# Kernel tuning notes

Measured on AMD Instinct MI355X. Metric: run time of the kernel, lower is better.

## Reference

```python
import jax, jax.numpy as jnp
import numpy as np

T, B, F, H, A, MH = 512, 256, 512, 128, 8, 64


def setup_inputs() -> dict:
    key = jax.random.key(0)
    ks = jax.random.split(key, 14)
    s = 0.05
    return {
        "x": jax.random.normal(ks[0], (T, B, F), dtype=jnp.float32),
        "done": (jax.random.uniform(ks[1], (T, B)) < 0.1).astype(jnp.float32),
        "h0": jnp.zeros((B, H), dtype=jnp.float32),
        "c0": jnp.zeros((B, H), dtype=jnp.float32),
        "W_ih": jax.random.normal(ks[2], (4 * H, F), dtype=jnp.float32) * s,
        "W_hh": jax.random.normal(ks[3], (4 * H, H), dtype=jnp.float32) * s,
        "b_ih": jnp.zeros((4 * H,), dtype=jnp.float32),
        "b_hh": jnp.zeros((4 * H,), dtype=jnp.float32),
        "W_p1": jax.random.normal(ks[4], (H, MH), dtype=jnp.float32) * s,
        "b_p1": jnp.zeros((MH,), dtype=jnp.float32),
        "W_p2": jax.random.normal(ks[5], (MH, A), dtype=jnp.float32) * s,
        "b_p2": jnp.zeros((A,), dtype=jnp.float32),
        "W_v1": jax.random.normal(ks[6], (H, MH), dtype=jnp.float32) * s,
        "b_v1": jnp.zeros((MH,), dtype=jnp.float32),
        "W_v2": jax.random.normal(ks[7], (MH, 1), dtype=jnp.float32) * s,
        "b_v2": jnp.zeros((1,), dtype=jnp.float32),
    }


def _masked_lstm(x, done, h0, c0, W_ih, W_hh, b_ih, b_hh):
    # Per-timestep LSTM with done-mask reset, as in MemoryAgent.remember().
    def step(carry, inp):
        h, c = carry
        xt, dt = inp  # xt: [B,F], dt: [B]
        m = (1.0 - dt)[:, None]
        h = h * m
        c = c * m
        gates = xt @ W_ih.T + b_ih + h @ W_hh.T + b_hh  # [B,4H]
        i, f, g, o = jnp.split(gates, 4, axis=-1)  # PyTorch gate order i,f,g,o
        i = jax.nn.sigmoid(i)
        f = jax.nn.sigmoid(f)
        g = jnp.tanh(g)
        o = jax.nn.sigmoid(o)
        c = f * c + i * g
        h = o * jnp.tanh(c)
        return (h, c), h

    (hT, cT), hs = jax.lax.scan(step, (h0, c0), (x, done))
    return hs.reshape(-1, h0.shape[-1]), hT, cT  # [T*B,H]


def reference(x, done, h0, c0, W_ih, W_hh, b_ih, b_hh,
              W_p1, b_p1, W_p2, b_p2, W_v1, b_v1, W_v2, b_v2):
    hseq, hT, cT = _masked_lstm(x, done, h0, c0, W_ih, W_hh, b_ih, b_hh)
    logits = jnp.tanh(hseq @ W_p1 + b_p1) @ W_p2 + b_p2  # [T*B,A]
    v = jnp.tanh(hseq @ W_v1 + b_v1) @ W_v2 + b_v2        # [T*B,1]
    out = jnp.concatenate([logits, v], axis=1)            # [T*B,A+1]
    return out, hT, cT
```

## Files before the change

### kernel.cpp

```cpp
#include <hip/hip_runtime.h>
#include <stdint.h>

#define T_  512
#define B_  256
#define F_  512
#define H_  128
#define MH_ 64
#define A_  8
#define OUT0 1179648
#define OUT1 32768

typedef float f32x4 __attribute__((ext_vector_type(4)));
typedef __bf16 bfrag8 __attribute__((ext_vector_type(8)));
typedef unsigned short u16;
typedef unsigned int u32;

#define WS_GATES 0u
#define WS_HSEQ  134217728u
#define WS_WIH   167772160u
#define WS_WHH   168296448u
#define WS_WP1   168427520u
#define WS_WV1   168443904u

__device__ inline u16 f2bf(float f) {
  union { float f; u32 u; } v; v.f = f;
  u32 u = v.u;
  u32 r = (u + 0x7FFFu + ((u >> 16) & 1u)) >> 16;
  return (u16)r;
}
__device__ inline float bf2f(u16 b) {
  union { u32 u; float f; } v; v.u = ((u32)b) << 16;
  return v.f;
}

__device__ inline float fexp2(float x) {
#if __has_builtin(__builtin_amdgcn_exp2f)
  return __builtin_amdgcn_exp2f(x);
#else
  return exp2f(x);
#endif
}
__device__ inline float frcp(float x) {
#if __has_builtin(__builtin_amdgcn_rcpf)
  return __builtin_amdgcn_rcpf(x);
#else
  return 1.0f / x;
#endif
}
__device__ inline float sig_(float x) {
  return frcp(1.0f + fexp2(-1.44269504f * x));
}
__device__ inline float tanh_(float x) {
  x = fminf(30.0f, fmaxf(-30.0f, x));
  float t = fexp2(2.88539008f * x);
  return (t - 1.0f) * frcp(t + 1.0f);
}
__device__ inline float sel4(f32x4 a, int q) {
  float s01 = (q & 1) ? a[1] : a[0];
  float s23 = (q & 1) ? a[3] : a[2];
  return (q & 2) ? s23 : s01;
}

__device__ inline f32x4 mfma16(bfrag8 a, bfrag8 b, f32x4 c) {
  return __builtin_amdgcn_mfma_f32_16x16x32_bf16(a, b, c, 0, 0, 0);
}

__device__ inline void gld16(const void* g, void* l) {
  __builtin_amdgcn_global_load_lds((const __attribute__((address_space(1))) void*)g,
                                   (__attribute__((address_space(3))) void*)l, 16, 0, 0);
}

__global__ __launch_bounds__(256) void k0_prep(const float* __restrict__ W_ih,
                                               const float* __restrict__ W_hh,
                                               const float* __restrict__ W_p1,
                                               const float* __restrict__ W_v1,
                                               u16* __restrict__ wih_swz,
                                               u16* __restrict__ whh_bf,
                                               u16* __restrict__ wp1s,
                                               u16* __restrict__ wv1s) {
  int idx = blockIdx.x * 256 + threadIdx.x;
  if (idx < 262144) {
    int i = idx & 7, L = (idx >> 3) & 63, kb = (idx >> 9) & 15, nt = idx >> 13;
    wih_swz[idx] = f2bf(W_ih[(nt * 16 + (L & 15)) * 512 + kb * 32 + ((L >> 4) << 3) + i]);
  } else if (idx < 262144 + 65536) {
    int j = idx - 262144;
    whh_bf[j] = f2bf(W_hh[j]);
  } else if (idx < 262144 + 65536 + 8192) {
    int j = idx - (262144 + 65536);
    int i = j & 7, L = (j >> 3) & 63, kb = (j >> 9) & 3, nt = j >> 11;
    wp1s[j] = f2bf(W_p1[(kb * 32 + ((L >> 4) << 3) + i) * 64 + nt * 16 + (L & 15)]);
  } else if (idx < 262144 + 65536 + 16384) {
    int j = idx - (262144 + 65536 + 8192);
    int i = j & 7, L = (j >> 3) & 63, kb = (j >> 9) & 3, nt = j >> 11;
    wv1s[j] = f2bf(W_v1[(kb * 32 + ((L >> 4) << 3) + i) * 64 + nt * 16 + (L & 15)]);
  }
}

__global__ __launch_bounds__(512) void k1_gates(const float* __restrict__ x,
                                                const u16* __restrict__ wih_swz,
                                                const float* __restrict__ b_ih,
                                                const float* __restrict__ b_hh,
                                                u16* __restrict__ gates) {
  __shared__ __align__(16) u16 Abuf[16 * 64 * 8];
  __shared__ __align__(16) u16 Bbuf[64 * 64 * 8];
  const int tid = threadIdx.x;
  const int lane = tid & 63;
  const int w = tid >> 6;
  const int lrow = lane >> 4, lcol = lane & 15;
  const int m0 = blockIdx.x * 128;
  const int mt0 = (w & 1) * 4, nt0 = (w >> 1) * 8;
  f32x4 acc[4][8] = {};

  for (int k0 = 0; k0 < 512; k0 += 64) {
#pragma unroll
    for (int cc = 0; cc < 8; ++cc) {
      int c = w * 8 + cc;
      int ntg = c >> 1;
      int kbg = (k0 >> 5) + (c & 1);
      gld16(wih_swz + (ntg * 16 + kbg) * 512 + lane * 8, &Bbuf[c * 512]);
    }
#pragma unroll
    for (int j = 0; j < 4; ++j) {
      int s = tid + 512 * j;
      int c = s >> 7, L = (s >> 1) & 63, hh = s & 1;
      int mt = c >> 1, kb = c & 1;
      const float4 v = *(const float4*)&x[(m0 + mt * 16 + (L & 15)) * 512 +
                                          k0 + kb * 32 + ((L >> 4) << 3) + hh * 4];
      ushort4 pk;
      pk.x = f2bf(v.x); pk.y = f2bf(v.y); pk.z = f2bf(v.z); pk.w = f2bf(v.w);
      *(ushort4*)&Abuf[(c * 64 + L) * 8 + hh * 4] = pk;
    }
    __syncthreads();
#pragma unroll
    for (int kk = 0; kk < 2; ++kk) {
      bfrag8 af[4], bfr[8];
#pragma unroll
      for (int im = 0; im < 4; ++im)
        af[im] = *(const bfrag8*)&Abuf[(((mt0 + im) * 2 + kk) * 64 + lane) * 8];
#pragma unroll
      for (int in = 0; in < 8; ++in)
        bfr[in] = *(const bfrag8*)&Bbuf[(((nt0 + in) * 2 + kk) * 64 + lane) * 8];
#pragma unroll
      for (int im = 0; im < 4; ++im)
#pragma unroll
        for (int in = 0; in < 8; ++in)
          acc[im][in] = mfma16(af[im], bfr[in], acc[im][in]);
    }
    __syncthreads();
  }
#pragma unroll
  for (int in = 0; in < 8; ++in) {
    int n = (nt0 + in) * 16 + lcol;
    float bias = b_ih[n] + b_hh[n];
#pragma unroll
    for (int im = 0; im < 4; ++im) {
      int mbase = m0 + (mt0 + im) * 16 + lrow * 4;
#pragma unroll
      for (int r = 0; r < 4; ++r)
        gates[(mbase + r) * 512 + n] = f2bf(acc[im][in][r] + bias);
    }
  }
}

__global__ __launch_bounds__(512) void k2_lstm(const float* __restrict__ done,
                                               const float* __restrict__ h0,
                                               const float* __restrict__ c0,
                                               const u16* __restrict__ whh_bf,
                                               const u16* __restrict__ gates,
                                               u16* __restrict__ hseq,
                                               float* __restrict__ dout) {
  __shared__ __align__(16) u16 h_lds[2][4][136];
  const int tid = threadIdx.x;
  const int lane = tid & 63;
  const int w = tid >> 6;
  const int lrow = lane >> 4, lcol = lane & 15;
  const int bbase = blockIdx.x * 4;
  const int jb = w * 16;
  const int q = lcol >> 2;
  const int bt = lcol & 3;
  const int hc = jb + lrow * 4 + q;
  const int brow = bbase + bt;

  bfrag8 wf[4][4];
#pragma unroll
  for (int g = 0; g < 4; ++g)
#pragma unroll
    for (int kk = 0; kk < 4; ++kk)
      wf[g][kk] = *(const bfrag8*)&whh_bf[(g * 128 + jb + lcol) * 128 + kk * 32 + lrow * 8];

  const float m0v = 1.0f - done[brow];
  h_lds[0][bt][hc] = f2bf(h0[brow * 128 + hc] * m0v);
  float c = c0[brow * 128 + hc] * m0v;
  float hfin = 0.0f;

  u32 gp[4], gpn[4];
#pragma unroll
  for (int g = 0; g < 4; ++g)
    gp[g] = gates[brow * 512 + g * 128 + hc];
  float dnx = done[B_ + brow];
  float dn2;

  for (int t = 0; t < T_; ++t) {
    const int cur = t & 1, nxt = cur ^ 1;
    __syncthreads();

    const int tn = (t + 1 < T_) ? t + 1 : T_ - 1;
    const int t2 = (t + 2 < T_) ? t + 2 : T_ - 1;
#pragma unroll
    for (int g = 0; g < 4; ++g)
      gpn[g] = gates[(tn * B_ + brow) * 512 + g * 128 + hc];
    dn2 = done[t2 * B_ + brow];
    const float live = (t < T_ - 1) ? 1.0f : 0.0f;
    const float mk = 1.0f - live * dnx;

    bfrag8 hf[4];
#pragma unroll
    for (int kk = 0; kk < 4; ++kk)
      hf[kk] = *(const bfrag8*)&h_lds[cur][bt][kk * 32 + lrow * 8];

    f32x4 acc[4] = {};
#pragma unroll
    for (int kk = 0; kk < 4; ++kk)
#pragma unroll
      for (int g = 0; g < 4; ++g)
        acc[g] = mfma16(wf[g][kk], hf[kk], acc[g]);

    float pi = sel4(acc[0], q) + bf2f((u16)gp[0]);
    float pf = sel4(acc[1], q) + bf2f((u16)gp[1]);
    float pg = sel4(acc[2], q) + bf2f((u16)gp[2]);
    float po = sel4(acc[3], q) + bf2f((u16)gp[3]);
    float iv = sig_(pi), fv = sig_(pf), gv = tanh_(pg), ov = sig_(po);
    float cc = fv * c + iv * gv;
    float hh = ov * tanh_(cc);
    c = cc * mk;
    hfin = hh;
    hseq[((t * B_ + brow) << 7) + hc] = f2bf(hh);
    h_lds[nxt][bt][hc] = f2bf(hh * mk);

#pragma unroll
    for (int g = 0; g < 4; ++g) gp[g] = gpn[g];
    dnx = dn2;
  }
  dout[OUT0 + brow * 128 + hc] = hfin;
  dout[OUT0 + OUT1 + brow * 128 + hc] = c;
}

__global__ __launch_bounds__(256) void k3_heads(const u16* __restrict__ hseq,
                                                const u16* __restrict__ wp1s,
                                                const u16* __restrict__ wv1s,
                                                const float* __restrict__ b_p1,
                                                const float* __restrict__ W_p2,
                                                const float* __restrict__ b_p2,
                                                const float* __restrict__ b_v1,
                                                const float* __restrict__ W_v2,
                                                const float* __restrict__ b_v2,
                                                float* __restrict__ out) {
  __shared__ float midp[4][16][68];
  __shared__ float midv[4][16][68];
  __shared__ float wsm[585];
  const int tid = threadIdx.x;
  const int lane = tid & 63, w = tid >> 6;
  const int lrow = lane >> 4, lcol = lane & 15;
  const int r0 = blockIdx.x * 64;

  for (int e = tid; e < 585; e += 256) {
    float v;
    if (e < 512) v = W_p2[e];
    else if (e < 576) v = W_v2[e - 512];
    else if (e < 584) v = b_p2[e - 576];
    else v = b_v2[0];
    wsm[e] = v;
  }

  const int rowA = r0 + w * 16 + lcol;
  bfrag8 af[4];
#pragma unroll
  for (int kk = 0; kk < 4; ++kk)
    af[kk] = *(const bfrag8*)&hseq[rowA * 128 + kk * 32 + lrow * 8];

#pragma unroll
  for (int nt = 0; nt < 4; ++nt) {
    f32x4 ap = {}, av = {};
#pragma unroll
    for (int kk = 0; kk < 4; ++kk) {
      ap = mfma16(af[kk], *(const bfrag8*)&wp1s[((nt * 4 + kk) * 64 + lane) * 8], ap);
      av = mfma16(af[kk], *(const bfrag8*)&wv1s[((nt * 4 + kk) * 64 + lane) * 8], av);
    }
    float bp = b_p1[nt * 16 + lcol], bv = b_v1[nt * 16 + lcol];
#pragma unroll
    for (int r = 0; r < 4; ++r) {
      midp[w][lrow * 4 + r][nt * 16 + lcol] = tanh_(ap[r] + bp);
      midv[w][lrow * 4 + r][nt * 16 + lcol] = tanh_(av[r] + bv);
    }
  }
  __syncthreads();

  for (int o = tid; o < 576; o += 256) {
    int row = o / 9;
    int a = o - row * 9;
    float s;
    if (a < 8) {
      s = wsm[576 + a];
      const float* mrow = &midp[row >> 4][row & 15][0];
#pragma unroll
      for (int n = 0; n < 64; ++n) s += mrow[n] * wsm[n * 8 + a];
    } else {
      s = wsm[584];
      const float* mrow = &midv[row >> 4][row & 15][0];
#pragma unroll
      for (int n = 0; n < 64; ++n) s += mrow[n] * wsm[512 + n];
    }
    out[(r0 + row) * 9 + a] = s;
  }
}

extern "C" void kernel_launch(void* const* d_in, const int* in_sizes, int n_in,
                              void* d_out, int out_size, void* d_ws, size_t ws_size,
                              hipStream_t stream) {
  const float* x    = (const float*)d_in[0];
  const float* done = (const float*)d_in[1];
  const float* h0   = (const float*)d_in[2];
  const float* c0   = (const float*)d_in[3];
  const float* W_ih = (const float*)d_in[4];
  const float* W_hh = (const float*)d_in[5];
  const float* b_ih = (const float*)d_in[6];
  const float* b_hh = (const float*)d_in[7];
  const float* W_p1 = (const float*)d_in[8];
  const float* b_p1 = (const float*)d_in[9];
  const float* W_p2 = (const float*)d_in[10];
  const float* b_p2 = (const float*)d_in[11];
  const float* W_v1 = (const float*)d_in[12];
  const float* b_v1 = (const float*)d_in[13];
  const float* W_v2 = (const float*)d_in[14];
  const float* b_v2 = (const float*)d_in[15];

  char* ws = (char*)d_ws;
  u16* gates   = (u16*)(ws + WS_GATES);
  u16* hseq    = (u16*)(ws + WS_HSEQ);
  u16* wih_swz = (u16*)(ws + WS_WIH);
  u16* whh_bf  = (u16*)(ws + WS_WHH);
  u16* wp1s    = (u16*)(ws + WS_WP1);
  u16* wv1s    = (u16*)(ws + WS_WV1);
  float* out = (float*)d_out;

  k0_prep<<<dim3(1344), dim3(256), 0, stream>>>(W_ih, W_hh, W_p1, W_v1,
                                                wih_swz, whh_bf, wp1s, wv1s);
  k1_gates<<<dim3(1024), dim3(512), 0, stream>>>(x, wih_swz, b_ih, b_hh, gates);
  k2_lstm<<<dim3(64), dim3(512), 0, stream>>>(done, h0, c0, whh_bf, gates, hseq, out);
  k3_heads<<<dim3(2048), dim3(256), 0, stream>>>(hseq, wp1s, wv1s, b_p1, W_p2, b_p2,
                                                 b_v1, W_v2, b_v2, out);
}
```

Baseline: 837.7 us.

## Re-layout gates to MFMA-fragment order and deepen LSTM prefetch with lighter barrier

```diff
diff --git a/kernel.cpp b/kernel.cpp
--- a/kernel.cpp
+++ b/kernel.cpp
@@ -51,9 +51,8 @@
   return frcp(1.0f + fexp2(-1.44269504f * x));
 }
 __device__ inline float tanh_(float x) {
-  x = fminf(30.0f, fmaxf(-30.0f, x));
   float t = fexp2(2.88539008f * x);
-  return (t - 1.0f) * frcp(t + 1.0f);
+  return 1.0f - 2.0f * frcp(t + 1.0f);
 }
 __device__ inline float sel4(f32x4 a, int q) {
   float s01 = (q & 1) ? a[1] : a[0];
@@ -68,6 +67,10 @@
 __device__ inline void gld16(const void* g, void* l) {
   __builtin_amdgcn_global_load_lds((const __attribute__((address_space(1))) void*)g,
                                    (__attribute__((address_space(3))) void*)l, 16, 0, 0);
+}
+
+__device__ inline void lds_barrier() {
+  __asm__ __volatile__("s_waitcnt lgkmcnt(0)\n\ts_barrier" ::: "memory");
 }
 
 __global__ __launch_bounds__(256) void k0_prep(const float* __restrict__ W_ih,
@@ -106,7 +109,7 @@
   const int tid = threadIdx.x;
   const int lane = tid & 63;
   const int w = tid >> 6;
-  const int lrow = lane >> 4, lcol = lane & 15;
+  const int lcol = lane & 15;
   const int m0 = blockIdx.x * 128;
   const int mt0 = (w & 1) * 4, nt0 = (w >> 1) * 8;
   f32x4 acc[4][8] = {};
@@ -121,14 +124,15 @@
     }
 #pragma unroll
     for (int j = 0; j < 4; ++j) {
-      int s = tid + 512 * j;
-      int c = s >> 7, L = (s >> 1) & 63, hh = s & 1;
-      int mt = c >> 1, kb = c & 1;
-      const float4 v = *(const float4*)&x[(m0 + mt * 16 + (L & 15)) * 512 +
-                                          k0 + kb * 32 + ((L >> 4) << 3) + hh * 4];
+      int idx = tid + 512 * j;
+      int row = idx >> 4, pos = idx & 15;
+      const float4 v = *(const float4*)&x[(m0 + row) * 512 + k0 + pos * 4];
+      int c = (row >> 4) * 2 + (pos >> 3);
+      int L = (row & 15) + ((pos & 7) >> 1) * 16;
+      int i = (pos & 1) * 4;
       ushort4 pk;
       pk.x = f2bf(v.x); pk.y = f2bf(v.y); pk.z = f2bf(v.z); pk.w = f2bf(v.w);
-      *(ushort4*)&Abuf[(c * 64 + L) * 8 + hh * 4] = pk;
+      *(ushort4*)&Abuf[(c * 64 + L) * 8 + i] = pk;
     }
     __syncthreads();
 #pragma unroll
@@ -148,16 +152,20 @@
     }
     __syncthreads();
   }
+  u32* gd = (u32*)gates;
 #pragma unroll
   for (int in = 0; in < 8; ++in) {
     int n = (nt0 + in) * 16 + lcol;
     float bias = b_ih[n] + b_hh[n];
 #pragma unroll
     for (int im = 0; im < 4; ++im) {
-      int mbase = m0 + (mt0 + im) * 16 + lrow * 4;
-#pragma unroll
-      for (int r = 0; r < 4; ++r)
-        gates[(mbase + r) * 512 + n] = f2bf(acc[im][in][r] + bias);
+      int chunk = (blockIdx.x * 8 + mt0 + im) * 32 + in * 4 + (w >> 1);
+#pragma unroll
+      for (int rp = 0; rp < 2; ++rp) {
+        u32 lo = f2bf(acc[im][in][2 * rp] + bias);
+        u32 hi = f2bf(acc[im][in][2 * rp + 1] + bias);
+        gd[(chunk * 2 + rp) * 64 + lane] = lo | (hi << 16);
+      }
     }
   }
 }
@@ -169,7 +177,7 @@
                                                const u16* __restrict__ gates,
                                                u16* __restrict__ hseq,
                                                float* __restrict__ dout) {
-  __shared__ __align__(16) u16 h_lds[2][4][136];
+  __shared__ __align__(16) u16 hbuf[2048];
   const int tid = threadIdx.x;
   const int lane = tid & 63;
   const int w = tid >> 6;
@@ -181,6 +189,15 @@
   const int hc = jb + lrow * 4 + q;
   const int brow = bbase + bt;
 
+  const int mt_b = (bbase & 127) >> 4;
+  const int mlrow = (bbase >> 2) & 3;
+  const int rp = bt >> 1, rl = bt & 1;
+  const int chunk0 = ((bbase >> 7) * 8 + mt_b) * 32 + w * 4;
+  const int goff = (chunk0 * 2 + rp) * 128 + (mlrow * 16 + lrow * 4 + q) * 2 + rl;
+  const int soff = brow * 128 + hc;
+  const int rdc = bt * 144 + lrow * 8;
+  const int wrc = bt * 144 + hc;
+
   bfrag8 wf[4][4];
 #pragma unroll
   for (int g = 0; g < 4; ++g)
@@ -189,34 +206,39 @@
       wf[g][kk] = *(const bfrag8*)&whh_bf[(g * 128 + jb + lcol) * 128 + kk * 32 + lrow * 8];
 
   const float m0v = 1.0f - done[brow];
-  h_lds[0][bt][hc] = f2bf(h0[brow * 128 + hc] * m0v);
+  hbuf[wrc] = f2bf(h0[brow * 128 + hc] * m0v);
   float c = c0[brow * 128 + hc] * m0v;
-  float hfin = 0.0f;
-
-  u32 gp[4], gpn[4];
-#pragma unroll
-  for (int g = 0; g < 4; ++g)
-    gp[g] = gates[brow * 512 + g * 128 + hc];
+  float hh = 0.0f;
+  u16 hb_prev = 0;
+
+  u32 gp[4], gpn[4], gpn2[4];
+  {
+    const u16* g0 = gates + goff;
+#pragma unroll
+    for (int g = 0; g < 4; ++g) gp[g] = g0[g * 256];
+    const u16* g1 = gates + 131072 + goff;
+#pragma unroll
+    for (int g = 0; g < 4; ++g) gpn[g] = g1[g * 256];
+  }
   float dnx = done[B_ + brow];
   float dn2;
 
   for (int t = 0; t < T_; ++t) {
-    const int cur = t & 1, nxt = cur ^ 1;
-    __syncthreads();
-
-    const int tn = (t + 1 < T_) ? t + 1 : T_ - 1;
-    const int t2 = (t + 2 < T_) ? t + 2 : T_ - 1;
-#pragma unroll
-    for (int g = 0; g < 4; ++g)
-      gpn[g] = gates[(tn * B_ + brow) * 512 + g * 128 + hc];
-    dn2 = done[t2 * B_ + brow];
-    const float live = (t < T_ - 1) ? 1.0f : 0.0f;
-    const float mk = 1.0f - live * dnx;
-
+    lds_barrier();
+
+    if (t) hseq[(size_t)(t - 1) * 32768 + soff] = hb_prev;
+
+    const int tg = (t + 2 < T_) ? t + 2 : T_ - 1;
+    const u16* gb = gates + (size_t)tg * 131072 + goff;
+#pragma unroll
+    for (int g = 0; g < 4; ++g) gpn2[g] = gb[g * 256];
+    dn2 = done[tg * B_ + brow];
+
+    const u16* hp = hbuf + rdc + ((t & 1) << 10);
     bfrag8 hf[4];
 #pragma unroll
     for (int kk = 0; kk < 4; ++kk)
-      hf[kk] = *(const bfrag8*)&h_lds[cur][bt][kk * 32 + lrow * 8];
+      hf[kk] = *(const bfrag8*)(hp + kk * 32);
 
     f32x4 acc[4] = {};
 #pragma unroll
@@ -231,18 +253,20 @@
     float po = sel4(acc[3], q) + bf2f((u16)gp[3]);
     float iv = sig_(pi), fv = sig_(pf), gv = tanh_(pg), ov = sig_(po);
     float cc = fv * c + iv * gv;
-    float hh = ov * tanh_(cc);
-    c = cc * mk;
-    hfin = hh;
-    hseq[((t * B_ + brow) << 7) + hc] = f2bf(hh);
-    h_lds[nxt][bt][hc] = f2bf(hh * mk);
-
-#pragma unroll
-    for (int g = 0; g < 4; ++g) gp[g] = gpn[g];
+    hh = ov * tanh_(cc);
+    bool rs = (dnx != 0.0f) && (t < T_ - 1);
+    c = rs ? 0.0f : cc;
+    u16 hb = f2bf(hh);
+    hbuf[wrc + (((t & 1) ^ 1) << 10)] = rs ? (u16)0 : hb;
+    hb_prev = hb;
+
+#pragma unroll
+    for (int g = 0; g < 4; ++g) { gp[g] = gpn[g]; gpn[g] = gpn2[g]; }
     dnx = dn2;
   }
-  dout[OUT0 + brow * 128 + hc] = hfin;
-  dout[OUT0 + OUT1 + brow * 128 + hc] = c;
+  hseq[(size_t)(T_ - 1) * 32768 + soff] = hb_prev;
+  dout[OUT0 + soff] = hh;
+  dout[OUT0 + OUT1 + soff] = c;
 }
 
 __global__ __launch_bounds__(256) void k3_heads(const u16* __restrict__ hseq,
```

After: 947.2 us. 1.13x slower.
